# Kernel optimization log

Measured on AMD Instinct MI355X. Metric: run time of the kernel, lower is better.

Reference implementation:

```python
import jax, jax.numpy as jnp
from jax import lax
import numpy as np

DN = ('NCDHW', 'OIDHW', 'NCDHW')
ACTIVE_THRESH = 1


def setup_inputs() -> dict:
    key = jax.random.key(0)
    ks = jax.random.split(key, 10)
    B, D = 4, 64
    chans = [3, 64, 128, 256, 512]
    inp = {
        'x': jax.random.normal(ks[0], (B, 3, D, D, D), jnp.float32),
        'mask': jax.random.randint(ks[1], (B, D, D, D), 0, 20, jnp.int32),
    }
    for i in range(4):
        cin, cout = chans[i], chans[i + 1]
        fan_in = cin * 27
        scale = 1.0 / np.sqrt(fan_in)
        inp[f'w{i+1}'] = jax.random.normal(ks[2 + 2 * i], (cout, cin, 3, 3, 3), jnp.float32) * scale
        inp[f'b{i+1}'] = jax.random.normal(ks[3 + 2 * i], (cout,), jnp.float32) * scale
    return inp


def _sparse_block(x, m, w, b, stride):
    # SparseConv3d(k=3, pad=1) + SparseReLU: output active where 3^3 footprint hits an active input;
    # bias + relu applied only at active sites, inactive sites stay exactly 0 (spconv .dense() semantics).
    s = (stride,) * 3
    pad = [(1, 1)] * 3
    y = lax.conv_general_dilated(x, w, s, pad, dimension_numbers=DN)
    ones = jnp.ones((1, 1, 3, 3, 3), x.dtype)
    m_out = lax.conv_general_dilated(m[:, None].astype(x.dtype), ones, s, pad, dimension_numbers=DN) > 0
    y = jnp.where(m_out, jax.nn.relu(y + b[None, :, None, None, None]), jnp.zeros((), x.dtype))
    return y, m_out[:, 0]


def reference(x, mask, w1, b1, w2, b2, w3, b3, w4, b4):
    m = mask < ACTIVE_THRESH                       # [B,D,H,W] active voxels
    h = x * m[:, None].astype(x.dtype)             # zero inactive input features
    h, m = _sparse_block(h, m, w1, b1, 1)          # [B,64,64,64,64]
    h, m = _sparse_block(h, m, w2, b2, 2)          # [B,128,32,32,32]
    h, m = _sparse_block(h, m, w3, b3, 2)          # [B,256,16,16,16]
    h, m = _sparse_block(h, m, w4, b4, 2)          # [B,512,8,8,8]
    pooled = jnp.max(h, axis=(2, 3, 4))            # dense() + amax over D,H,W -> [B,512]
    return jax.nn.leaky_relu(pooled, negative_slope=0.2)
```

## Files before the change

### kernel.cpp

```cpp
#include <hip/hip_runtime.h>

typedef _Float16 f16;
typedef _Float16 half4 __attribute__((ext_vector_type(4)));
typedef _Float16 half8 __attribute__((ext_vector_type(8)));
typedef float f32x4 __attribute__((ext_vector_type(4)));

#define BATCH 4

__device__ __forceinline__ void gload16(const void* g, void* l) {
  __builtin_amdgcn_global_load_lds((const __attribute__((address_space(1))) unsigned int*)g,
                                   (__attribute__((address_space(3))) unsigned int*)l, 16, 0, 0);
}

template<int DP, int ROWB>
__device__ __forceinline__ void zb_one(char* __restrict__ buf, int v, int b) {
  int w = v % DP; int t = v / DP; int h = t % DP; int d = t / DP;
  bool border = (w == 0) | (w == DP - 1) | (h == 0) | (h == DP - 1) | (d == 0) | (d == DP - 1);
  if (!border) return;
  char* p = buf + ((size_t)b * DP * DP * DP + v) * ROWB;
  #pragma unroll
  for (int i = 0; i < ROWB; i += 8)
    *reinterpret_cast<unsigned long long*>(p + i) = 0ull;
}

template<int DP, int ROWB>
__global__ __launch_bounds__(256) void zborder_k(char* __restrict__ buf) {
  int v = blockIdx.x * 256 + threadIdx.x;
  if (v >= DP * DP * DP) return;
  zb_one<DP, ROWB>(buf, v, blockIdx.y);
}

__global__ __launch_bounds__(256) void zb12_k(char* __restrict__ h1p, char* __restrict__ h2p) {
  const int N1 = 66 * 66 * 66, N2 = 34 * 34 * 34;
  int idx = blockIdx.x * 256 + threadIdx.x;
  int b = blockIdx.y;
  if (idx < N1) { zb_one<66, 128>(h1p, idx, b); return; }
  idx -= N1;
  if (idx < N2) zb_one<34, 256>(h2p, idx, b);
}

__global__ __launch_bounds__(256) void wprep_all_k(const float* __restrict__ w1,
                                                   const float* __restrict__ w2,
                                                   const float* __restrict__ w3,
                                                   const float* __restrict__ w4,
                                                   f16* __restrict__ wf1,
                                                   f16* __restrict__ wf2,
                                                   f16* __restrict__ wf3,
                                                   f16* __restrict__ wf4) {
  const int T1 = 64 * 128;
  const int T2 = 27 * 128 * 64;
  const int T3 = 27 * 256 * 128;
  const int T4 = 27 * 512 * 256;
  int idx = blockIdx.x * 256 + threadIdx.x;
  if (idx < T1) {
    int q = idx & 127, co = idx >> 7;
    int k = q >> 2, ci = q & 3;
    float v = (ci < 3 && k < 27) ? w1[(co * 3 + ci) * 27 + k] : 0.f;
    wf1[idx] = (f16)v;
    return;
  }
  idx -= T1;
  const float* w; f16* wo; int COUT, CIN;
  if (idx < T2)       { w = w2; wo = wf2; COUT = 128; CIN = 64; }
  else if ((idx -= T2) < T3) { w = w3; wo = wf3; COUT = 256; CIN = 128; }
  else if ((idx -= T3) < T4) { w = w4; wo = wf4; COUT = 512; CIN = 256; }
  else return;
  int k = idx % 27;
  int t = idx / 27;
  int ci = t % CIN;
  int co = t / CIN;
  wo[((size_t)k * COUT + co) * CIN + ci] = (f16)w[idx];
}

__global__ __launch_bounds__(256) void xmask_k(const float* __restrict__ x,
                                               const int* __restrict__ mask,
                                               f16* __restrict__ xcp) {
  const int D3 = 262144, PD = 66, PD3 = PD * PD * PD;
  int pv = blockIdx.x * 256 + threadIdx.x;
  if (pv >= PD3) return;
  int b = blockIdx.y;
  int pw = pv % PD; int t = pv / PD; int ph = t % PD; int pd = t / PD;
  half4 o = {};
  if (pw > 0 && pw < 65 && ph > 0 && ph < 65 && pd > 0 && pd < 65) {
    int v = (((pd - 1) * 64) + (ph - 1)) * 64 + (pw - 1);
    bool act = mask[(size_t)b * D3 + v] < 1;
    if (act) {
      const float* xb = x + (size_t)b * 3 * D3 + v;
      o[0] = (f16)xb[0];
      o[1] = (f16)xb[D3];
      o[2] = (f16)xb[2 * D3];
    }
  }
  *reinterpret_cast<half4*>(xcp + ((size_t)b * PD3 + pv) * 4) = o;
}

__global__ __launch_bounds__(256) void dil_w_k(const int* __restrict__ mask,
                                               unsigned char* __restrict__ aw) {
  const int D3 = 262144;
  int t = blockIdx.x * 256 + threadIdx.x;
  int b = t >> 16;
  int v = (t & 65535) * 4;
  int w0 = v & 63;
  const int* mb = mask + (size_t)b * D3;
  int a[6];
  a[0] = (w0 > 0) ? (mb[v - 1] < 1) : 0;
  #pragma unroll
  for (int i = 0; i < 4; i++) a[i + 1] = mb[v + i] < 1;
  a[5] = (w0 < 60) ? (mb[v + 4] < 1) : 0;
  unsigned int o = 0;
  #pragma unroll
  for (int i = 0; i < 4; i++)
    o |= ((unsigned)(a[i] | a[i + 1] | a[i + 2])) << (8 * i);
  *reinterpret_cast<unsigned int*>(aw + (size_t)b * D3 + v) = o;
}

__global__ __launch_bounds__(256) void dil_hd2_k(const unsigned char* __restrict__ aw,
                                                 unsigned char* __restrict__ m1) {
  const int D3 = 262144;
  int t = blockIdx.x * 256 + threadIdx.x;
  int b = t >> 16;
  int v = (t & 65535) * 4;
  int h = (v >> 6) & 63;
  int d = v >> 12;
  const unsigned char* ib = aw + (size_t)b * D3;
  unsigned int m = 0;
  #pragma unroll
  for (int dd = -1; dd <= 1; dd++) {
    int id = d + dd; if ((unsigned)id >= 64u) continue;
    #pragma unroll
    for (int hh = -1; hh <= 1; hh++) {
      int ih = h + hh; if ((unsigned)ih >= 64u) continue;
      m |= *reinterpret_cast<const unsigned int*>(ib + ((id << 12) | (ih << 6) | (v & 63)));
    }
  }
  *reinterpret_cast<unsigned int*>(m1 + (size_t)b * D3 + v) = m;
}

__global__ __launch_bounds__(256) void dil_rest_k(const unsigned char* __restrict__ m1,
                                                  unsigned char* __restrict__ m2,
                                                  unsigned char* __restrict__ m3,
                                                  unsigned char* __restrict__ m4,
                                                  float* __restrict__ outp) {
  const int D = 64, D3 = 262144;
  const int S2 = BATCH * 32768, S3 = BATCH * 4096, S4 = BATCH * 512;
  int idx = blockIdx.x * 256 + threadIdx.x;
  int b, v, LOGD, H, ST;
  unsigned char* mo;
  if (idx < S2)                 { b = idx >> 15; v = idx & 32767; LOGD = 5; H = 1; ST = 2; mo = m2 + (size_t)b * 32768; }
  else if ((idx -= S2) < S3)    { b = idx >> 12; v = idx & 4095;  LOGD = 4; H = 3; ST = 4; mo = m3 + (size_t)b * 4096; }
  else if ((idx -= S3) < S4)    { b = idx >> 9;  v = idx & 511;   LOGD = 3; H = 7; ST = 8; mo = m4 + (size_t)b * 512; }
  else if ((idx -= S4) < 2048)  { outp[idx] = 0.f; return; }
  else return;
  int DM = (1 << LOGD) - 1;
  int ow = v & DM, oh = (v >> LOGD) & DM, od = v >> (2 * LOGD);
  const unsigned char* mb = m1 + (size_t)b * D3;
  int act = 0;
  for (int dd = -H; dd <= H && !act; dd++) {
    int id = od * ST + dd; if ((unsigned)id >= (unsigned)D) continue;
    for (int hh = -H; hh <= H && !act; hh++) {
      int ih = oh * ST + hh; if ((unsigned)ih >= (unsigned)D) continue;
      for (int ww = -H; ww <= H; ww++) {
        int iw = ow * ST + ww; if ((unsigned)iw >= (unsigned)D) continue;
        if (mb[((size_t)id * D + ih) * D + iw]) { act = 1; break; }
      }
    }
  }
  mo[v] = (unsigned char)act;
}

template<int BM>
__global__ __launch_bounds__(256) void conv1_mfma_k(const f16* __restrict__ xcp,
                                                    const f16* __restrict__ w1f,
                                                    const float* __restrict__ bias,
                                                    const unsigned char* __restrict__ mo,
                                                    f16* __restrict__ out ) {
  const int D3 = 262144, COUT = 64, PD = 66, PD3 = PD * PD * PD;
  constexpr int K = 128, LD = K + 8;
  constexpr int WM = 2, WN = 2;
  constexpr int MF = BM / (16 * WM), NF = 64 / (16 * WN);
  __shared__ __align__(16) f16 As[BM][LD];
  __shared__ __align__(16) f16 Bs[64][LD];

  const int tid = threadIdx.x, lane = tid & 63, wave = tid >> 6;
  const int wm = wave >> 1, wn = wave & 1;
  const int v0 = blockIdx.x * BM;
  const int b = blockIdx.y;
  const f16* xb = xcp + (size_t)b * PD3 * 4;

  for (int c = tid; c < 64 * (K / 8); c += 256) {
    int row = c >> 4, cc = c & 15;
    *reinterpret_cast<half8*>(&Bs[row][cc * 8]) =
        *reinterpret_cast<const half8*>(w1f + row * K + cc * 8);
  }
  {
    const int row = tid & (BM - 1);
    const int v = v0 + row;
    const int ow = v & 63, oh = (v >> 6) & 63, od = v >> 12;
    const int base = (od * PD + oh) * PD + ow;
    for (int e = tid; e < 32 * BM; e += 256) {
      int kslot = e / BM;
      half4 val = {};
      if (kslot < 27) {
        int kd = kslot / 9, r2 = kslot - kd * 9, kh = r2 / 3, kw = r2 - kh * 3;
        val = *reinterpret_cast<const half4*>(xb + (size_t)(base + (kd * PD + kh) * PD + kw) * 4);
      }
      *reinterpret_cast<half4*>(&As[row][kslot * 4]) = val;
    }
  }
  __syncthreads();

  f32x4 acc[MF][NF] = {};
  const int chanoff = (lane >> 4) << 3;
  const int arow = wm * MF * 16 + (lane & 15);
  const int brow = wn * NF * 16 + (lane & 15);
  #pragma unroll
  for (int q0 = 0; q0 < K; q0 += 32) {
    half8 a[MF], bb[NF];
    #pragma unroll
    for (int mf = 0; mf < MF; mf++)
      a[mf] = *reinterpret_cast<const half8*>(&As[arow + mf * 16][q0 + chanoff]);
    #pragma unroll
    for (int nf = 0; nf < NF; nf++)
      bb[nf] = *reinterpret_cast<const half8*>(&Bs[brow + nf * 16][q0 + chanoff]);
    #pragma unroll
    for (int mf = 0; mf < MF; mf++)
      #pragma unroll
      for (int nf = 0; nf < NF; nf++)
        acc[mf][nf] = __builtin_amdgcn_mfma_f32_16x16x32_f16(a[mf], bb[nf], acc[mf][nf], 0, 0, 0);
  }

  const unsigned char* mb = mo + (size_t)b * D3;
  f16* ob = out + (size_t)b * PD3 * COUT;
  const int ll = lane & 15, lh = lane >> 4;
  float bv[NF];
  #pragma unroll
  for (int nf = 0; nf < NF; nf++) bv[nf] = bias[wn * NF * 16 + nf * 16 + ll];
  #pragma unroll
  for (int mf = 0; mf < MF; mf++) {
    #pragma unroll
    for (int r = 0; r < 4; r++) {
      int v = v0 + wm * MF * 16 + mf * 16 + (lh << 2) + r;
      bool act = mb[v] != 0;
      int ow = v & 63, oh = (v >> 6) & 63, od = v >> 12;
      size_t pv = ((size_t)(od + 1) * PD + oh + 1) * PD + ow + 1;
      #pragma unroll
      for (int nf = 0; nf < NF; nf++) {
        int co = wn * NF * 16 + nf * 16 + ll;
        float val = acc[mf][nf][r] + bv[nf];
        val = act ? (val > 0.f ? val : 0.f) : 0.f;
        ob[pv * COUT + co] = (f16)val;
      }
    }
  }
}

template<int CINS, int CINF, int COUT, int DIN, int DOUT, int BM, int BN,
         int WM, int WN, int SWZ, int OP, int BMERGE, int POOL>
__global__ __launch_bounds__(WM * WN * 64) void conv_mfma2_k(const f16* __restrict__ in,
                                                             const f16* __restrict__ w27,
                                                             const float* __restrict__ bias,
                                                             const unsigned char* __restrict__ mo,
                                                             f16* __restrict__ out,
                                                             float* __restrict__ poolp) {
  constexpr int PD = DIN + 2, PDo = DOUT + 2;
  constexpr int NW = WM * WN;
  constexpr int MF = BM / (16 * WM), NF = BN / (16 * WN);
  constexpr int ROWB = CINS * 2;
  constexpr int ROWBF = CINF * 2;
  constexpr int CHUNKS = ROWB / 16;
  constexpr int RPI = 64 / CHUNKS;
  constexpr int A_IW = BM / RPI / NW;
  constexpr int B_IW = BN / RPI / NW;
  constexpr int CIH = CINF / CINS;
  constexpr int NSTEP = 27 * CIH;
  constexpr int CI0S = CINS / 32;
  constexpr int D3o = DOUT * DOUT * DOUT;
  constexpr int LOGD = (DOUT == 32) ? 5 : ((DOUT == 16) ? 4 : 3);

  __shared__ __align__(16) char As[2][BM * ROWB];
  __shared__ __align__(16) char Bs[2][BN * ROWB];

  const int tid = threadIdx.x, lane = tid & 63, wave = tid >> 6;
  const int wm = wave / WN, wn = wave % WN;
  int bx = blockIdx.x;
  if (SWZ) {
    int cpx = gridDim.x >> 3;
    bx = (bx & 7) * cpx + (bx >> 3);
  }
  const int v0 = bx * BM, co0 = blockIdx.y * BN;
  const int bz = BMERGE ? 0 : blockIdx.z;

  auto key = [](int r) -> int { return (CHUNKS >= 8) ? (r & 7) : ((r >> 1) & 3); };

  const int lrow = lane / CHUNKS;
  const int lchunk = lane % CHUNKS;
  const char* a_src[A_IW];
  #pragma unroll
  for (int i = 0; i < A_IW; i++) {
    int r = (wave * A_IW + i) * RPI + lrow;
    int v = v0 + r;
    int vb = BMERGE ? (v >> (3 * LOGD)) : bz;
    int vv = BMERGE ? (v & (D3o - 1)) : v;
    int ow = vv & (DOUT - 1), oh = (vv >> LOGD) & (DOUT - 1), od = vv >> (2 * LOGD);
    size_t flat = (size_t)vb * PD * PD * PD + ((size_t)(2 * od) * PD + 2 * oh) * PD + 2 * ow;
    a_src[i] = (const char*)in + flat * ROWBF + (lchunk ^ key(r)) * 16;
  }
  const char* b_src[B_IW];
  #pragma unroll
  for (int i = 0; i < B_IW; i++) {
    int r = (wave * B_IW + i) * RPI + lrow;
    b_src[i] = (const char*)w27 + (size_t)(co0 + r) * ROWBF + (lchunk ^ key(r)) * 16;
  }

  auto stage = [&](int buf, int s) {
    int k = s / CIH;
    int h = s - k * CIH;
    int kd = k / 9, r2 = k - kd * 9, kh = r2 / 3, kw = r2 - kh * 3;
    int koff = ((kd * PD + kh) * PD + kw) * ROWBF + h * ROWB;
    #pragma unroll
    for (int i = 0; i < A_IW; i++)
      gload16(a_src[i] + koff, &As[buf][(wave * A_IW + i) * 1024]);
    size_t wko = (size_t)k * COUT * ROWBF + h * ROWB;
    #pragma unroll
    for (int i = 0; i < B_IW; i++)
      gload16(b_src[i] + wko, &Bs[buf][(wave * B_IW + i) * 1024]);
  };

  f32x4 acc[MF][NF] = {};
  const int ll = lane & 15, lh = lane >> 4;
  const int ra0 = wm * MF * 16 + ll;
  const int rb0 = wn * NF * 16 + ll;
  const int rswa = key(ra0);
  const int rswb = key(rb0);

  stage(0, 0);
  __syncthreads();
  int cur = 0;
  for (int s = 0; s < NSTEP; s++) {
    if (s < NSTEP - 1) stage(cur ^ 1, s + 1);
    #pragma unroll
    for (int c = 0; c < CI0S; c++) {
      const int q = c * 4 + lh;
      half8 a[MF], bb[NF];
      #pragma unroll
      for (int mf = 0; mf < MF; mf++)
        a[mf] = *reinterpret_cast<const half8*>(
            &As[cur][(ra0 + mf * 16) * ROWB + ((q ^ rswa) * 16)]);
      #pragma unroll
      for (int nf = 0; nf < NF; nf++)
        bb[nf] = *reinterpret_cast<const half8*>(
            &Bs[cur][(rb0 + nf * 16) * ROWB + ((q ^ rswb) * 16)]);
      #pragma unroll
      for (int mf = 0; mf < MF; mf++)
        #pragma unroll
        for (int nf = 0; nf < NF; nf++)
          acc[mf][nf] = __builtin_amdgcn_mfma_f32_16x16x32_f16(a[mf], bb[nf], acc[mf][nf], 0, 0, 0);
    }
    __syncthreads();
    cur ^= 1;
  }

  f16* ob = out;
  float bv[NF];
  #pragma unroll
  for (int nf = 0; nf < NF; nf++) bv[nf] = bias[co0 + wn * NF * 16 + nf * 16 + ll];
  float pmax[NF];
  #pragma unroll
  for (int nf = 0; nf < NF; nf++) pmax[nf] = 0.f;
  #pragma unroll
  for (int mf = 0; mf < MF; mf++) {
    #pragma unroll
    for (int r = 0; r < 4; r++) {
      int v = v0 + wm * MF * 16 + mf * 16 + (lh << 2) + r;
      int vb = BMERGE ? (v >> (3 * LOGD)) : bz;
      int vv = BMERGE ? (v & (D3o - 1)) : v;
      bool act = mo[(size_t)vb * D3o + vv] != 0;
      int ow = vv & (DOUT - 1), oh = (vv >> LOGD) & (DOUT - 1), od = vv >> (2 * LOGD);
      size_t pv = OP ? (((size_t)(od + 1) * PDo + oh + 1) * PDo + ow + 1) : (size_t)vv;
      size_t obase = ((size_t)vb * (OP ? PDo * PDo * PDo : D3o) + pv) * COUT;
      #pragma unroll
      for (int nf = 0; nf < NF; nf++) {
        int co = co0 + wn * NF * 16 + nf * 16 + ll;
        float val = acc[mf][nf][r] + bv[nf];
        val = act ? (val > 0.f ? val : 0.f) : 0.f;
        if constexpr (POOL) {
          pmax[nf] = fmaxf(pmax[nf], val);
        } else {
          ob[obase + co] = (f16)val;
        }
      }
    }
  }
  if constexpr (POOL) {
    #pragma unroll
    for (int nf = 0; nf < NF; nf++) {
      int co = co0 + wn * NF * 16 + nf * 16 + ll;
      atomicMax((int*)poolp + bz * 512 + co, __float_as_int(pmax[nf]));
    }
  }
}

extern "C" void kernel_launch(void* const* d_in, const int* in_sizes, int n_in,
                              void* d_out, int out_size, void* d_ws, size_t ws_size,
                              hipStream_t stream) {
  const float* x    = (const float*)d_in[0];
  const int*   mask = (const int*)d_in[1];
  const float* w1 = (const float*)d_in[2];
  const float* b1 = (const float*)d_in[3];
  const float* w2 = (const float*)d_in[4];
  const float* b2 = (const float*)d_in[5];
  const float* w3 = (const float*)d_in[6];
  const float* b3 = (const float*)d_in[7];
  const float* w4 = (const float*)d_in[8];
  const float* b4 = (const float*)d_in[9];
  float* outp = (float*)d_out;

  const size_t PD1 = 66 * 66 * 66;
  const size_t PD2 = 34 * 34 * 34;
  const size_t PD3s = 18 * 18 * 18;

  char* ws = (char*)d_ws;
  size_t off = 0;
  auto alloc = [&](size_t bytes) -> char* {
    char* p = ws + off;
    off = (off + bytes + 255) & ~(size_t)255;
    return p;
  };
  f16* wf1 = (f16*)alloc((size_t)64 * 128 * 2);
  f16* wf2 = (f16*)alloc((size_t)27 * 128 * 64 * 2);
  f16* wf3 = (f16*)alloc((size_t)27 * 256 * 128 * 2);
  f16* wf4 = (f16*)alloc((size_t)27 * 512 * 256 * 2);
  unsigned char* aw = (unsigned char*)alloc((size_t)BATCH * 262144);
  unsigned char* m1 = (unsigned char*)alloc((size_t)BATCH * 262144);
  unsigned char* m2 = (unsigned char*)alloc((size_t)BATCH * 32768);
  unsigned char* m3 = (unsigned char*)alloc((size_t)BATCH * 4096);
  unsigned char* m4 = (unsigned char*)alloc((size_t)BATCH * 512);
  f16* h1p = (f16*)alloc((size_t)BATCH * PD1 * 64 * 2);
  f16* h2p = (f16*)alloc((size_t)BATCH * PD2 * 128 * 2);
  f16* h3p = (f16*)alloc((size_t)BATCH * PD3s * 256 * 2);
  f16* xcp = h3p;
  if (off > ws_size) return;

  {
    const int TOT = 64 * 128 + 27 * 128 * 64 + 27 * 256 * 128 + 27 * 512 * 256;
    wprep_all_k<<<dim3((TOT + 255) / 256), 256, 0, stream>>>(w1, w2, w3, w4, wf1, wf2, wf3, wf4);
  }

  dil_w_k<<<dim3(BATCH * 65536 / 256), 256, 0, stream>>>(mask, aw);
  dil_hd2_k<<<dim3(BATCH * 65536 / 256), 256, 0, stream>>>(aw, m1);
  {
    const int TOT = BATCH * 32768 + BATCH * 4096 + BATCH * 512 + 2048;
    dil_rest_k<<<dim3((TOT + 255) / 256), 256, 0, stream>>>(m1, m2, m3, m4, outp);
  }

  xmask_k<<<dim3((287496 + 255) / 256, BATCH), 256, 0, stream>>>(x, mask, xcp);
  zb12_k<<<dim3((287496 + 39304 + 255) / 256, BATCH), 256, 0, stream>>>((char*)h1p, (char*)h2p);

  conv1_mfma_k<128><<<dim3(262144 / 128, BATCH), 256, 0, stream>>>(xcp, wf1, b1, m1, h1p);

  zborder_k<18, 512><<<dim3((5832 + 255) / 256, BATCH), 256, 0, stream>>>((char*)h3p);

  conv_mfma2_k<64, 64, 128, 64, 32, 64, 128, 2, 2, 1, 1, 0, 0>
      <<<dim3(512, 1, BATCH), 256, 0, stream>>>(h1p, wf2, b2, m2, h2p, nullptr);
  conv_mfma2_k<64, 128, 256, 32, 16, 64, 128, 2, 2, 1, 1, 1, 0>
      <<<dim3(256, 2, 1), 256, 0, stream>>>(h2p, wf3, b3, m3, h3p, nullptr);
  conv_mfma2_k<128, 256, 512, 16, 8, 32, 64, 1, 2, 0, 0, 0, 1>
      <<<dim3(16, 8, BATCH), 128, 0, stream>>>(h3p, wf4, b4, m4, nullptr, outp);
}
```

Baseline: 324.6 us.

## Build conv1 A-operand from a shared halo tile and fuse prep kernels

conv1 no longer builds a fully im2col'd A tile in LDS. It loads a 3x4x66 halo slab of padded input once per block and forms the MFMA A fragments by indexing into it with per-lane tap offsets, which cuts global gathers and LDS writes. The xmask and three border-zeroing kernels are merged into one launch. Because of that, xcp gets its own workspace buffer instead of aliasing h3p, since h3p's border is now zeroed in the same launch. The cost is extra workspace and possible LDS bank conflicts on the half4 halo reads.

```diff
diff --git a/kernel.cpp b/kernel.cpp
--- a/kernel.cpp
+++ b/kernel.cpp
@@ -21,22 +21,6 @@
   #pragma unroll
   for (int i = 0; i < ROWB; i += 8)
     *reinterpret_cast<unsigned long long*>(p + i) = 0ull;
-}
-
-template<int DP, int ROWB>
-__global__ __launch_bounds__(256) void zborder_k(char* __restrict__ buf) {
-  int v = blockIdx.x * 256 + threadIdx.x;
-  if (v >= DP * DP * DP) return;
-  zb_one<DP, ROWB>(buf, v, blockIdx.y);
-}
-
-__global__ __launch_bounds__(256) void zb12_k(char* __restrict__ h1p, char* __restrict__ h2p) {
-  const int N1 = 66 * 66 * 66, N2 = 34 * 34 * 34;
-  int idx = blockIdx.x * 256 + threadIdx.x;
-  int b = blockIdx.y;
-  if (idx < N1) { zb_one<66, 128>(h1p, idx, b); return; }
-  idx -= N1;
-  if (idx < N2) zb_one<34, 256>(h2p, idx, b);
 }
 
 __global__ __launch_bounds__(256) void wprep_all_k(const float* __restrict__ w1,
@@ -72,26 +56,38 @@
   wo[((size_t)k * COUT + co) * CIN + ci] = (f16)w[idx];
 }
 
-__global__ __launch_bounds__(256) void xmask_k(const float* __restrict__ x,
-                                               const int* __restrict__ mask,
-                                               f16* __restrict__ xcp) {
+__global__ __launch_bounds__(256) void prep_all_k(const float* __restrict__ x,
+                                                  const int* __restrict__ mask,
+                                                  f16* __restrict__ xcp,
+                                                  char* __restrict__ h1p,
+                                                  char* __restrict__ h2p,
+                                                  char* __restrict__ h3p) {
   const int D3 = 262144, PD = 66, PD3 = PD * PD * PD;
-  int pv = blockIdx.x * 256 + threadIdx.x;
-  if (pv >= PD3) return;
+  const int N3 = 34 * 34 * 34, N4 = 18 * 18 * 18;
+  int idx = blockIdx.x * 256 + threadIdx.x;
   int b = blockIdx.y;
-  int pw = pv % PD; int t = pv / PD; int ph = t % PD; int pd = t / PD;
-  half4 o = {};
-  if (pw > 0 && pw < 65 && ph > 0 && ph < 65 && pd > 0 && pd < 65) {
-    int v = (((pd - 1) * 64) + (ph - 1)) * 64 + (pw - 1);
-    bool act = mask[(size_t)b * D3 + v] < 1;
-    if (act) {
-      const float* xb = x + (size_t)b * 3 * D3 + v;
-      o[0] = (f16)xb[0];
-      o[1] = (f16)xb[D3];
-      o[2] = (f16)xb[2 * D3];
-    }
-  }
-  *reinterpret_cast<half4*>(xcp + ((size_t)b * PD3 + pv) * 4) = o;
+  if (idx < PD3) {
+    int pv = idx;
+    int pw = pv % PD; int t = pv / PD; int ph = t % PD; int pd = t / PD;
+    half4 o = {};
+    if (pw > 0 && pw < 65 && ph > 0 && ph < 65 && pd > 0 && pd < 65) {
+      int v = (((pd - 1) * 64) + (ph - 1)) * 64 + (pw - 1);
+      if (mask[(size_t)b * D3 + v] < 1) {
+        const float* xb = x + (size_t)b * 3 * D3 + v;
+        o[0] = (f16)xb[0];
+        o[1] = (f16)xb[D3];
+        o[2] = (f16)xb[2 * D3];
+      }
+    }
+    *reinterpret_cast<half4*>(xcp + ((size_t)b * PD3 + pv) * 4) = o;
+    return;
+  }
+  idx -= PD3;
+  if (idx < PD3) { zb_one<66, 128>(h1p, idx, b); return; }
+  idx -= PD3;
+  if (idx < N3) { zb_one<34, 256>(h2p, idx, b); return; }
+  idx -= N3;
+  if (idx < N4) zb_one<18, 512>(h3p, idx, b);
 }
 
 __global__ __launch_bounds__(256) void dil_w_k(const int* __restrict__ mask,
@@ -175,16 +171,17 @@
                                                     const unsigned char* __restrict__ mo,
                                                     f16* __restrict__ out ) {
   const int D3 = 262144, COUT = 64, PD = 66, PD3 = PD * PD * PD;
-  constexpr int K = 128, LD = K + 8;
+  constexpr int K = 128, LDB = K + 8;
   constexpr int WM = 2, WN = 2;
   constexpr int MF = BM / (16 * WM), NF = 64 / (16 * WN);
-  __shared__ __align__(16) f16 As[BM][LD];
-  __shared__ __align__(16) f16 Bs[64][LD];
+  __shared__ __align__(16) f16 halo[1056 * 4];
+  __shared__ __align__(16) f16 Bs[64][LDB];
 
   const int tid = threadIdx.x, lane = tid & 63, wave = tid >> 6;
   const int wm = wave >> 1, wn = wave & 1;
   const int v0 = blockIdx.x * BM;
   const int b = blockIdx.y;
+  const int oh0 = (v0 >> 6) & 63, od = v0 >> 12;
   const f16* xb = xcp + (size_t)b * PD3 * 4;
 
   for (int c = tid; c < 64 * (K / 8); c += 256) {
@@ -192,36 +189,40 @@
     *reinterpret_cast<half8*>(&Bs[row][cc * 8]) =
         *reinterpret_cast<const half8*>(w1f + row * K + cc * 8);
   }
-  {
-    const int row = tid & (BM - 1);
-    const int v = v0 + row;
-    const int ow = v & 63, oh = (v >> 6) & 63, od = v >> 12;
-    const int base = (od * PD + oh) * PD + ow;
-    for (int e = tid; e < 32 * BM; e += 256) {
-      int kslot = e / BM;
-      half4 val = {};
-      if (kslot < 27) {
-        int kd = kslot / 9, r2 = kslot - kd * 9, kh = r2 / 3, kw = r2 - kh * 3;
-        val = *reinterpret_cast<const half4*>(xb + (size_t)(base + (kd * PD + kh) * PD + kw) * 4);
-      }
-      *reinterpret_cast<half4*>(&As[row][kslot * 4]) = val;
-    }
+  for (int e = tid; e < 1056; e += 256) {
+    half4 val = {};
+    if (e < 792) {
+      int d = e / 264, r = e - d * 264, h = r / 66, w = r - h * 66;
+      val = *reinterpret_cast<const half4*>(
+          xb + (((size_t)(od + d) * PD + (oh0 + h)) * PD + w) * 4);
+    }
+    *reinterpret_cast<half4*>(&halo[(size_t)e * 4]) = val;
   }
   __syncthreads();
 
+  const int ll = lane & 15, lh = lane >> 4;
+  int koff[8];
+  #pragma unroll
+  for (int i = 0; i < 8; i++) {
+    int ks = (i >> 1) * 8 + 2 * lh + (i & 1);
+    int kd = ks / 9, rr = ks - kd * 9, kh = rr / 3, kw = rr - kh * 3;
+    koff[i] = ((kd * 4 + kh) * 66 + kw) * 4;
+  }
+  const int lbase = (wm * 66 + ll) * 4;
+
   f32x4 acc[MF][NF] = {};
-  const int chanoff = (lane >> 4) << 3;
-  const int arow = wm * MF * 16 + (lane & 15);
-  const int brow = wn * NF * 16 + (lane & 15);
-  #pragma unroll
-  for (int q0 = 0; q0 < K; q0 += 32) {
+  #pragma unroll
+  for (int q = 0; q < 4; q++) {
     half8 a[MF], bb[NF];
     #pragma unroll
-    for (int mf = 0; mf < MF; mf++)
-      a[mf] = *reinterpret_cast<const half8*>(&As[arow + mf * 16][q0 + chanoff]);
+    for (int mf = 0; mf < MF; mf++) {
+      half4 lo = *reinterpret_cast<const half4*>(&halo[lbase + mf * 64 + koff[q * 2]]);
+      half4 hi = *reinterpret_cast<const half4*>(&halo[lbase + mf * 64 + koff[q * 2 + 1]]);
+      a[mf] = half8{lo[0], lo[1], lo[2], lo[3], hi[0], hi[1], hi[2], hi[3]};
+    }
     #pragma unroll
     for (int nf = 0; nf < NF; nf++)
-      bb[nf] = *reinterpret_cast<const half8*>(&Bs[brow + nf * 16][q0 + chanoff]);
+      bb[nf] = *reinterpret_cast<const half8*>(&Bs[wn * NF * 16 + nf * 16 + ll][q * 32 + lh * 8]);
     #pragma unroll
     for (int mf = 0; mf < MF; mf++)
       #pragma unroll
@@ -231,7 +232,6 @@
 
   const unsigned char* mb = mo + (size_t)b * D3;
   f16* ob = out + (size_t)b * PD3 * COUT;
-  const int ll = lane & 15, lh = lane >> 4;
   float bv[NF];
   #pragma unroll
   for (int nf = 0; nf < NF; nf++) bv[nf] = bias[wn * NF * 16 + nf * 16 + ll];
@@ -241,8 +241,8 @@
     for (int r = 0; r < 4; r++) {
       int v = v0 + wm * MF * 16 + mf * 16 + (lh << 2) + r;
       bool act = mb[v] != 0;
-      int ow = v & 63, oh = (v >> 6) & 63, od = v >> 12;
-      size_t pv = ((size_t)(od + 1) * PD + oh + 1) * PD + ow + 1;
+      int ow = v & 63, oh = (v >> 6) & 63, odv = v >> 12;
+      size_t pv = ((size_t)(odv + 1) * PD + oh + 1) * PD + ow + 1;
       #pragma unroll
       for (int nf = 0; nf < NF; nf++) {
         int co = wn * NF * 16 + nf * 16 + ll;
@@ -438,7 +438,7 @@
   f16* h1p = (f16*)alloc((size_t)BATCH * PD1 * 64 * 2);
   f16* h2p = (f16*)alloc((size_t)BATCH * PD2 * 128 * 2);
   f16* h3p = (f16*)alloc((size_t)BATCH * PD3s * 256 * 2);
-  f16* xcp = h3p;
+  f16* xcp = (f16*)alloc((size_t)BATCH * PD1 * 4 * 2);
   if (off > ws_size) return;
 
   {
@@ -453,12 +453,13 @@
     dil_rest_k<<<dim3((TOT + 255) / 256), 256, 0, stream>>>(m1, m2, m3, m4, outp);
   }
 
-  xmask_k<<<dim3((287496 + 255) / 256, BATCH), 256, 0, stream>>>(x, mask, xcp);
-  zb12_k<<<dim3((287496 + 39304 + 255) / 256, BATCH), 256, 0, stream>>>((char*)h1p, (char*)h2p);
+  {
+    const int TOT = 287496 * 2 + 39304 + 5832;
+    prep_all_k<<<dim3((TOT + 255) / 256, BATCH), 256, 0, stream>>>(
+        x, mask, xcp, (char*)h1p, (char*)h2p, (char*)h3p);
+  }
 
   conv1_mfma_k<128><<<dim3(262144 / 128, BATCH), 256, 0, stream>>>(xcp, wf1, b1, m1, h1p);
-
-  zborder_k<18, 512><<<dim3((5832 + 255) / 256, BATCH), 256, 0, stream>>>((char*)h3p);
 
   conv_mfma2_k<64, 64, 128, 64, 32, 64, 128, 2, 2, 1, 1, 0, 0>
       <<<dim3(512, 1, BATCH), 256, 0, stream>>>(h1p, wf2, b2, m2, h2p, nullptr);
```

Result: faster. 293.2 us (median of 2 runs) (-9.7%).
